# Optimization experiments

Measured on AMD Instinct MI355X. Metric: run time of the kernel, lower is better.

Reference implementation:

```python
import jax, jax.numpy as jnp
import numpy as np

NBITS = 8
REDUCE = 64
OUT = 512


def setup_inputs() -> dict:
    key = jax.random.key(0)
    ks = jax.random.split(key, 6)
    T, B, C = 512, 16, 512
    ne = 2 ** NBITS
    x = jax.random.normal(ks[0], (T, B, C), dtype=jnp.float32)
    key_in = jax.random.normal(ks[1], (T, B, C), dtype=jnp.float32)  # unused by forward (overwritten)
    # xavier-ish init scales
    map_w = jax.random.normal(ks[2], (NBITS, C), dtype=jnp.float32) * np.sqrt(2.0 / (C + NBITS))
    map_b = jnp.zeros((NBITS,), dtype=jnp.float32)
    pw_w1 = jax.random.normal(ks[3], (REDUCE, C), dtype=jnp.float32) * np.sqrt(2.0 / (C + REDUCE))
    pw_w21 = jax.random.normal(ks[4], (ne, OUT * REDUCE), dtype=jnp.float32) * np.sqrt(2.0 / (ne + OUT * REDUCE))
    pw_w22 = jax.random.normal(ks[5], (ne, OUT * REDUCE), dtype=jnp.float32) * np.sqrt(2.0 / (ne + OUT * REDUCE))
    pw_B = jnp.zeros((1, 1, OUT), dtype=jnp.float32)
    return {"x": x, "key": key_in, "map_w": map_w, "map_b": map_b,
            "pw_w1": pw_w1, "pw_w21": pw_w21, "pw_w22": pw_w22, "pw_B": pw_B}


def reference(x, key, map_w, map_b, pw_w1, pw_w21, pw_w22, pw_B):
    # x: (T,B,C). `key` arg is overwritten by x in the original source.
    T, B, C = x.shape
    nbits = map_w.shape[0]
    out_dim = pw_B.shape[-1]
    reduce_dim = pw_w1.shape[0]

    k = x.reshape(T * B, C) @ map_w.T + map_b          # (T*B, nbits)
    z = jnp.clip(1.2 * jax.nn.sigmoid(k) - 0.1, 0.0, 1.0)  # saturated sigmoid
    code = (z > 0.5).astype(z.dtype)                   # eval: hard binary code

    pows = (2 ** jnp.arange(nbits, dtype=jnp.int32))   # bit_to_int weights
    qz1 = jnp.sum(code.astype(jnp.int32) * pows, axis=-1)          # (T*B,)
    qz2 = jnp.sum((1 - code.astype(jnp.int32)) * pows, axis=-1)    # (T*B,)

    # gather per-token expert rows and synthesize per-token weight matrix
    w2 = (pw_w21[qz1] + pw_w22[qz2]).reshape(T, B, out_dim, reduce_dim)

    # original computes (w2 @ pw_w1) @ x; reassociated as w2 @ (pw_w1 @ x)
    # to avoid materializing the (T,B,out,in) intermediate (same math)
    v = jnp.einsum('ri,tbi->tbr', pw_w1, x)            # (T,B,reduce)
    y = jnp.einsum('tbor,tbr->tbo', w2, v) + pw_B      # (T,B,out)

    loss = jnp.zeros((1,), dtype=x.dtype)
    return (y, loss)
```

## Files before the change

kernel.cpp:

```cpp
#include <hip/hip_runtime.h>

#define NTOK 8192
#define CDIM 512
#define NB   8
#define RD   64
#define OD   512
#define XROW 516

typedef unsigned char  u8;
typedef unsigned int   u32;
typedef unsigned short u16;

#define WS_Q      0
#define WS_COUNTS 8192
#define WS_CURSOR 9216
#define WS_OFF    10240
#define WS_LIST   11520
#define WS_V      28672
#define WS_NEED   (WS_V + NTOK * RD * 4)

__global__ __launch_bounds__(256) void kInit(u32* __restrict__ counts) {
    counts[threadIdx.x] = 0u;
}

__global__ __launch_bounds__(256) void kA(
    const float* __restrict__ x, const float* __restrict__ map_w,
    const float* __restrict__ map_b, const float* __restrict__ w1,
    u8* __restrict__ q_out, float* __restrict__ v_out,
    u32* __restrict__ counts, float* __restrict__ loss_out)
{
    const int t    = threadIdx.x;
    const int tok0 = blockIdx.x * 16;
    __shared__ float xs[16 * XROW];

    const float4* __restrict__ xsrc = (const float4*)(x + (size_t)tok0 * CDIM);
    #pragma unroll
    for (int u = 0; u < 8; ++u) {
        int i = u * 256 + t;
        int r = i >> 7, c = i & 127;
        *(float4*)(xs + r * XROW + c * 4) = xsrc[i];
    }
    __syncthreads();

    const int wvu  = __builtin_amdgcn_readfirstlane(t >> 6);
    const int lane = t & 63;

    if (wvu < 2) {
        const int tb = tok0 + wvu * 8;
        const float4* __restrict__ w4  = (const float4*)w1 + (size_t)lane * 128;
        const float4* __restrict__ xg  = (const float4*)x + (size_t)tb * 128;
        float a0=0.f,a1=0.f,a2=0.f,a3=0.f,a4=0.f,a5=0.f,a6=0.f,a7=0.f;
        for (int k = 0; k < 128; ++k) {
            float4 w = w4[k];
            float4 x0 = xg[0*128+k], x1 = xg[1*128+k], x2 = xg[2*128+k], x3 = xg[3*128+k];
            float4 x4v = xg[4*128+k], x5 = xg[5*128+k], x6 = xg[6*128+k], x7 = xg[7*128+k];
            a0 += w.x*x0.x + w.y*x0.y + w.z*x0.z + w.w*x0.w;
            a1 += w.x*x1.x + w.y*x1.y + w.z*x1.z + w.w*x1.w;
            a2 += w.x*x2.x + w.y*x2.y + w.z*x2.z + w.w*x2.w;
            a3 += w.x*x3.x + w.y*x3.y + w.z*x3.z + w.w*x3.w;
            a4 += w.x*x4v.x + w.y*x4v.y + w.z*x4v.z + w.w*x4v.w;
            a5 += w.x*x5.x + w.y*x5.y + w.z*x5.z + w.w*x5.w;
            a6 += w.x*x6.x + w.y*x6.y + w.z*x6.z + w.w*x6.w;
            a7 += w.x*x7.x + w.y*x7.y + w.z*x7.z + w.w*x7.w;
        }
        v_out[(size_t)(tb+0) * RD + lane] = a0;
        v_out[(size_t)(tb+1) * RD + lane] = a1;
        v_out[(size_t)(tb+2) * RD + lane] = a2;
        v_out[(size_t)(tb+3) * RD + lane] = a3;
        v_out[(size_t)(tb+4) * RD + lane] = a4;
        v_out[(size_t)(tb+5) * RD + lane] = a5;
        v_out[(size_t)(tb+6) * RD + lane] = a6;
        v_out[(size_t)(tb+7) * RD + lane] = a7;
    } else {
        const int lt  = t - 128;
        const int tk  = lt >> 3;
        const int bit = lt & 7;
        const float4* __restrict__ m4 = (const float4*)map_w + (size_t)bit * 128;
        const float4* __restrict__ xl = (const float4*)(xs + tk * XROW);
        double s = 0.0;
        for (int k = 0; k < 128; ++k) {
            float4 m = m4[k], xv = xl[k];
            s += (double)m.x * (double)xv.x + (double)m.y * (double)xv.y
               + (double)m.z * (double)xv.z + (double)m.w * (double)xv.w;
        }
        s += (double)map_b[bit];
        unsigned long long mask = __ballot(s > 0.0);
        if (bit == 0) {
            u32 qv = (u32)((mask >> ((tk & 7) * 8)) & 0xFFull);
            q_out[tok0 + tk] = (u8)qv;
            atomicAdd(&counts[qv], 1u);
        }
    }
    if (blockIdx.x == 0 && t == 0) loss_out[0] = 0.0f;
}

__global__ __launch_bounds__(256) void kPrefix(
    const u32* __restrict__ counts, u32* __restrict__ off, u32* __restrict__ cursor)
{
    __shared__ u32 s[256];
    const int t = threadIdx.x;
    u32 c = counts[t];
    s[t] = c;
    __syncthreads();
    for (int d = 1; d < 256; d <<= 1) {
        u32 v = (t >= d) ? s[t - d] : 0u;
        __syncthreads();
        s[t] += v;
        __syncthreads();
    }
    u32 excl = s[t] - c;
    off[t] = excl;
    cursor[t] = excl;
    if (t == 255) off[256] = s[255];
}

__global__ __launch_bounds__(256) void kScatter(
    const u8* __restrict__ q_arr, u32* __restrict__ cursor, u16* __restrict__ list)
{
    const int tok = blockIdx.x * 256 + threadIdx.x;
    u32 pos = atomicAdd(&cursor[q_arr[tok]], 1u);
    list[pos] = (u16)tok;
}

__global__ __launch_bounds__(256) void kB(
    const u16* __restrict__ list, const u32* __restrict__ off,
    const float* __restrict__ v_arr,
    const float* __restrict__ w21, const float* __restrict__ w22,
    const float* __restrict__ pwB, float* __restrict__ y)
{
    const int q  = blockIdx.x >> 2;
    const int oh = (blockIdx.x >> 1) & 1;
    const int th = blockIdx.x & 1;
    const int t  = threadIdx.x;
    const int o  = oh * 256 + t;

    const u32 lo = off[q], hi = off[q + 1];
    const int n = (int)(hi - lo);
    if (n == 0) return;
    const int half = (n + 1) >> 1;
    const int s0   = th * half;
    const int cnt  = min(n - s0, half);
    if (cnt <= 0) return;

    __shared__ u16 ltok[4096];
    for (int i = t; i < cnt; i += 256) ltok[i] = list[lo + s0 + i];

    const float4* __restrict__ pa = (const float4*)(w21 + ((size_t)q * OD + o) * RD);
    const float4* __restrict__ pb = (const float4*)(w22 + ((size_t)(255 - q) * OD + o) * RD);
    float4 w[16];
    #pragma unroll
    for (int j = 0; j < 16; ++j) {
        float4 a = pa[j], b = pb[j];
        w[j] = make_float4(a.x + b.x, a.y + b.y, a.z + b.z, a.w + b.w);
    }
    const float bias = pwB[o];
    __syncthreads();

    const float4* __restrict__ v4 = (const float4*)v_arr;
    for (int i = 0; i < cnt; i += 4) {
        const int nb = cnt - i;
        const int i1 = (nb > 1) ? i + 1 : i;
        const int i2 = (nb > 2) ? i + 2 : i;
        const int i3 = (nb > 3) ? i + 3 : i;
        const int t0 = __builtin_amdgcn_readfirstlane((int)ltok[i]);
        const int t1 = __builtin_amdgcn_readfirstlane((int)ltok[i1]);
        const int t2 = __builtin_amdgcn_readfirstlane((int)ltok[i2]);
        const int t3 = __builtin_amdgcn_readfirstlane((int)ltok[i3]);
        const float4* __restrict__ p0 = v4 + (size_t)t0 * 16;
        const float4* __restrict__ p1 = v4 + (size_t)t1 * 16;
        const float4* __restrict__ p2 = v4 + (size_t)t2 * 16;
        const float4* __restrict__ p3 = v4 + (size_t)t3 * 16;
        float a0 = bias, a1 = bias, a2 = bias, a3 = bias;
        #pragma unroll
        for (int j = 0; j < 16; ++j) {
            float4 ww = w[j];
            float4 v0 = p0[j]; a0 += ww.x*v0.x + ww.y*v0.y + ww.z*v0.z + ww.w*v0.w;
            float4 v1 = p1[j]; a1 += ww.x*v1.x + ww.y*v1.y + ww.z*v1.z + ww.w*v1.w;
            float4 v2 = p2[j]; a2 += ww.x*v2.x + ww.y*v2.y + ww.z*v2.z + ww.w*v2.w;
            float4 v3 = p3[j]; a3 += ww.x*v3.x + ww.y*v3.y + ww.z*v3.z + ww.w*v3.w;
        }
        y[(size_t)t0 * OD + o] = a0;
        if (nb > 1) y[(size_t)t1 * OD + o] = a1;
        if (nb > 2) y[(size_t)t2 * OD + o] = a2;
        if (nb > 3) y[(size_t)t3 * OD + o] = a3;
    }
}

__global__ __launch_bounds__(256) void mono(
    const float* __restrict__ x, const float* __restrict__ map_w,
    const float* __restrict__ map_b, const float* __restrict__ w1,
    const float* __restrict__ w21, const float* __restrict__ w22,
    const float* __restrict__ pwB, float* __restrict__ y)
{
    const int tok = blockIdx.x;
    const int t   = threadIdx.x;
    __shared__ float xsh[CDIM];
    __shared__ float vsh[RD];
    __shared__ int qsh;

    if (t == 0) qsh = 0;
    for (int i = t; i < CDIM; i += 256) xsh[i] = x[(size_t)tok * CDIM + i];
    __syncthreads();

    if (t < NB) {
        double a = 0.0;
        const float* mrow = map_w + (size_t)t * CDIM;
        for (int j = 0; j < CDIM; ++j) a += (double)mrow[j] * (double)xsh[j];
        a += (double)map_b[t];
        if (a > 0.0) atomicOr(&qsh, 1 << t);
    }
    if (t < RD) {
        const float* wrow = w1 + (size_t)t * CDIM;
        float acc = 0.f;
        for (int j = 0; j < CDIM; ++j) acc += wrow[j] * xsh[j];
        vsh[t] = acc;
    }
    __syncthreads();

    const int q = qsh;
    for (int o = t; o < OD; o += 256) {
        const float* pa = w21 + (size_t)q * (OD * RD) + (size_t)o * RD;
        const float* pb = w22 + (size_t)(255 - q) * (OD * RD) + (size_t)o * RD;
        float acc = pwB[o];
        for (int r = 0; r < RD; ++r) acc += (pa[r] + pb[r]) * vsh[r];
        y[(size_t)tok * OD + o] = acc;
    }
    if (tok == 0 && t == 0) y[(size_t)NTOK * OD] = 0.0f;
}

extern "C" void kernel_launch(void* const* d_in, const int* in_sizes, int n_in,
                              void* d_out, int out_size, void* d_ws, size_t ws_size,
                              hipStream_t stream) {
    const float* x     = (const float*)d_in[0];
    const float* map_w = (const float*)d_in[2];
    const float* map_b = (const float*)d_in[3];
    const float* w1    = (const float*)d_in[4];
    const float* w21   = (const float*)d_in[5];
    const float* w22   = (const float*)d_in[6];
    const float* pwB   = (const float*)d_in[7];
    float* out = (float*)d_out;

    if (ws_size >= (size_t)WS_NEED) {
        char* ws = (char*)d_ws;
        u8*    q_ws   = (u8*)(ws + WS_Q);
        u32*   counts = (u32*)(ws + WS_COUNTS);
        u32*   cursor = (u32*)(ws + WS_CURSOR);
        u32*   off    = (u32*)(ws + WS_OFF);
        u16*   list   = (u16*)(ws + WS_LIST);
        float* v_ws   = (float*)(ws + WS_V);

        kInit<<<1, 256, 0, stream>>>(counts);
        kA<<<NTOK / 16, 256, 0, stream>>>(x, map_w, map_b, w1, q_ws, v_ws, counts,
                                          out + (size_t)NTOK * OD);
        kPrefix<<<1, 256, 0, stream>>>(counts, off, cursor);
        kScatter<<<NTOK / 256, 256, 0, stream>>>(q_ws, cursor, list);
        kB<<<1024, 256, 0, stream>>>(list, off, v_ws, w21, w22, pwB, out);
    } else {
        mono<<<NTOK, 256, 0, stream>>>(x, map_w, map_b, w1, w21, w22, pwB, out);
    }
}
```

Measured before the change: 223.4 us.

## Restructure projection kernel, merge histogram/scan/scatter into one sort kernel, reshape expert grid

The projection kernel now uses 512 threads with all 8 waves splitting both the w1 projection and the hash-code dot products. Each wave reads x from an XOR-swizzled shared tile and reduces its partial sums with cross-lane shuffles. The separate init, prefix and scatter kernels plus the global count atomics are replaced by a single one-block sort kernel that does the histogram, scan and scatter in shared memory. The expert kernel no longer splits tokens in halves, so it launches 512 blocks with a larger shared token list and issues weight loads early. This removes launches and global atomics, but serializes sorting in one block and gives uneven expert buckets less parallelism.

Result: slower. 232.9 us (+4.2%).

```diff
diff --git a/kernel.cpp b/kernel.cpp
--- a/kernel.cpp
+++ b/kernel.cpp
@@ -5,121 +5,125 @@
 #define NB   8
 #define RD   64
 #define OD   512
-#define XROW 516
 
 typedef unsigned char  u8;
 typedef unsigned int   u32;
 typedef unsigned short u16;
 
-#define WS_Q      0
-#define WS_COUNTS 8192
-#define WS_CURSOR 9216
-#define WS_OFF    10240
-#define WS_LIST   11520
-#define WS_V      28672
-#define WS_NEED   (WS_V + NTOK * RD * 4)
-
-__global__ __launch_bounds__(256) void kInit(u32* __restrict__ counts) {
-    counts[threadIdx.x] = 0u;
-}
-
-__global__ __launch_bounds__(256) void kA(
+#define WS_Q    0
+#define WS_OFF  8192
+#define WS_LIST 9728
+#define WS_V    26112
+#define WS_NEED (WS_V + (size_t)NTOK * RD * 4)
+
+__global__ __launch_bounds__(512) void kA(
     const float* __restrict__ x, const float* __restrict__ map_w,
     const float* __restrict__ map_b, const float* __restrict__ w1,
     u8* __restrict__ q_out, float* __restrict__ v_out,
-    u32* __restrict__ counts, float* __restrict__ loss_out)
+    float* __restrict__ loss_out)
 {
     const int t    = threadIdx.x;
     const int tok0 = blockIdx.x * 16;
-    __shared__ float xs[16 * XROW];
+    __shared__ float xs[16 * CDIM];
+    __shared__ float vs[16 * 68];
+    __shared__ u32   qm[8];
 
     const float4* __restrict__ xsrc = (const float4*)(x + (size_t)tok0 * CDIM);
     #pragma unroll
-    for (int u = 0; u < 8; ++u) {
-        int i = u * 256 + t;
-        int r = i >> 7, c = i & 127;
-        *(float4*)(xs + r * XROW + c * 4) = xsrc[i];
-    }
-    __syncthreads();
-
-    const int wvu  = __builtin_amdgcn_readfirstlane(t >> 6);
+    for (int u = 0; u < 4; ++u) {
+        int g  = u * 512 + t;
+        int r  = g >> 7, c4 = g & 127;
+        int col = (c4 * 4) ^ ((r & 7) << 3);
+        *(float4*)(xs + r * CDIM + col) = xsrc[g];
+    }
+    __syncthreads();
+
+    const int w    = t >> 6;
     const int lane = t & 63;
-
-    if (wvu < 2) {
-        const int tb = tok0 + wvu * 8;
-        const float4* __restrict__ w4  = (const float4*)w1 + (size_t)lane * 128;
-        const float4* __restrict__ xg  = (const float4*)x + (size_t)tb * 128;
-        float a0=0.f,a1=0.f,a2=0.f,a3=0.f,a4=0.f,a5=0.f,a6=0.f,a7=0.f;
-        for (int k = 0; k < 128; ++k) {
-            float4 w = w4[k];
-            float4 x0 = xg[0*128+k], x1 = xg[1*128+k], x2 = xg[2*128+k], x3 = xg[3*128+k];
-            float4 x4v = xg[4*128+k], x5 = xg[5*128+k], x6 = xg[6*128+k], x7 = xg[7*128+k];
-            a0 += w.x*x0.x + w.y*x0.y + w.z*x0.z + w.w*x0.w;
-            a1 += w.x*x1.x + w.y*x1.y + w.z*x1.z + w.w*x1.w;
-            a2 += w.x*x2.x + w.y*x2.y + w.z*x2.z + w.w*x2.w;
-            a3 += w.x*x3.x + w.y*x3.y + w.z*x3.z + w.w*x3.w;
-            a4 += w.x*x4v.x + w.y*x4v.y + w.z*x4v.z + w.w*x4v.w;
-            a5 += w.x*x5.x + w.y*x5.y + w.z*x5.z + w.w*x5.w;
-            a6 += w.x*x6.x + w.y*x6.y + w.z*x6.z + w.w*x6.w;
-            a7 += w.x*x7.x + w.y*x7.y + w.z*x7.z + w.w*x7.w;
+    const int tok  = lane & 15;
+    const int ch   = lane >> 4;
+    const int sw   = (tok & 7) << 3;
+    const float* __restrict__ xrow = xs + tok * CDIM;
+    const float* __restrict__ wrow = w1 + (size_t)(w * 8) * CDIM;
+    const float* __restrict__ mrow = map_w + (size_t)w * CDIM;
+
+    float a[8] = {0.f, 0.f, 0.f, 0.f, 0.f, 0.f, 0.f, 0.f};
+    double s = 0.0;
+
+    for (int st = 0; st < 32; ++st) {
+        const int c = ch * 128 + st * 4;
+        float4 xv = *(const float4*)(xrow + (c ^ sw));
+        #pragma unroll
+        for (int j = 0; j < 8; ++j) {
+            float4 wv = *(const float4*)(wrow + (size_t)j * CDIM + c);
+            a[j] += wv.x * xv.x + wv.y * xv.y + wv.z * xv.z + wv.w * xv.w;
         }
-        v_out[(size_t)(tb+0) * RD + lane] = a0;
-        v_out[(size_t)(tb+1) * RD + lane] = a1;
-        v_out[(size_t)(tb+2) * RD + lane] = a2;
-        v_out[(size_t)(tb+3) * RD + lane] = a3;
-        v_out[(size_t)(tb+4) * RD + lane] = a4;
-        v_out[(size_t)(tb+5) * RD + lane] = a5;
-        v_out[(size_t)(tb+6) * RD + lane] = a6;
-        v_out[(size_t)(tb+7) * RD + lane] = a7;
-    } else {
-        const int lt  = t - 128;
-        const int tk  = lt >> 3;
-        const int bit = lt & 7;
-        const float4* __restrict__ m4 = (const float4*)map_w + (size_t)bit * 128;
-        const float4* __restrict__ xl = (const float4*)(xs + tk * XROW);
-        double s = 0.0;
-        for (int k = 0; k < 128; ++k) {
-            float4 m = m4[k], xv = xl[k];
-            s += (double)m.x * (double)xv.x + (double)m.y * (double)xv.y
-               + (double)m.z * (double)xv.z + (double)m.w * (double)xv.w;
-        }
-        s += (double)map_b[bit];
-        unsigned long long mask = __ballot(s > 0.0);
-        if (bit == 0) {
-            u32 qv = (u32)((mask >> ((tk & 7) * 8)) & 0xFFull);
-            q_out[tok0 + tk] = (u8)qv;
-            atomicAdd(&counts[qv], 1u);
-        }
+        float4 mv = *(const float4*)(mrow + c);
+        s += (double)mv.x * (double)xv.x + (double)mv.y * (double)xv.y
+           + (double)mv.z * (double)xv.z + (double)mv.w * (double)xv.w;
+    }
+
+    #pragma unroll
+    for (int j = 0; j < 8; ++j) {
+        a[j] += __shfl_xor(a[j], 16);
+        a[j] += __shfl_xor(a[j], 32);
+    }
+    s += __shfl_xor(s, 16);
+    s += __shfl_xor(s, 32);
+    s += (double)map_b[w];
+
+    unsigned long long mask = __ballot(s > 0.0);
+    if (lane == 0) qm[w] = (u32)(mask & 0xFFFFull);
+
+    if (lane < 16) {
+        #pragma unroll
+        for (int j = 0; j < 8; ++j) vs[tok * 68 + w * 8 + j] = a[j];
+    }
+    __syncthreads();
+
+    if (t < 16) {
+        u32 q = 0;
+        #pragma unroll
+        for (int b = 0; b < 8; ++b) q |= ((qm[b] >> t) & 1u) << b;
+        q_out[tok0 + t] = (u8)q;
+    }
+    if (t < 256) {
+        int tk = t >> 4, j4 = t & 15;
+        *(float4*)(v_out + (size_t)(tok0 + tk) * RD + j4 * 4) =
+            *(const float4*)(vs + tk * 68 + j4 * 4);
     }
     if (blockIdx.x == 0 && t == 0) loss_out[0] = 0.0f;
 }
 
-__global__ __launch_bounds__(256) void kPrefix(
-    const u32* __restrict__ counts, u32* __restrict__ off, u32* __restrict__ cursor)
-{
-    __shared__ u32 s[256];
+__global__ __launch_bounds__(1024) void kSort(
+    const u8* __restrict__ q_arr, u32* __restrict__ off, u16* __restrict__ list)
+{
+    __shared__ u32 hist[256], curs[256], scan[256];
     const int t = threadIdx.x;
-    u32 c = counts[t];
-    s[t] = c;
+    if (t < 256) hist[t] = 0u;
+    __syncthreads();
+    for (int i = t; i < NTOK; i += 1024) atomicAdd(&hist[q_arr[i]], 1u);
+    __syncthreads();
+    if (t < 256) scan[t] = hist[t];
     __syncthreads();
     for (int d = 1; d < 256; d <<= 1) {
-        u32 v = (t >= d) ? s[t - d] : 0u;
+        u32 v = 0u;
+        if (t < 256 && t >= d) v = scan[t - d];
         __syncthreads();
-        s[t] += v;
+        if (t < 256) scan[t] += v;
         __syncthreads();
     }
-    u32 excl = s[t] - c;
-    off[t] = excl;
-    cursor[t] = excl;
-    if (t == 255) off[256] = s[255];
-}
-
-__global__ __launch_bounds__(256) void kScatter(
-    const u8* __restrict__ q_arr, u32* __restrict__ cursor, u16* __restrict__ list)
-{
-    const int tok = blockIdx.x * 256 + threadIdx.x;
-    u32 pos = atomicAdd(&cursor[q_arr[tok]], 1u);
-    list[pos] = (u16)tok;
+    if (t < 256) {
+        u32 excl = scan[t] - hist[t];
+        curs[t] = excl;
+        off[t]  = excl;
+        if (t == 255) off[256] = scan[255];
+    }
+    __syncthreads();
+    for (int i = t; i < NTOK; i += 1024) {
+        u32 pos = atomicAdd(&curs[q_arr[i]], 1u);
+        list[pos] = (u16)i;
+    }
 }
 
 __global__ __launch_bounds__(256) void kB(
@@ -128,44 +132,41 @@
     const float* __restrict__ w21, const float* __restrict__ w22,
     const float* __restrict__ pwB, float* __restrict__ y)
 {
-    const int q  = blockIdx.x >> 2;
-    const int oh = (blockIdx.x >> 1) & 1;
-    const int th = blockIdx.x & 1;
+    const int q  = blockIdx.x >> 1;
+    const int oh = blockIdx.x & 1;
     const int t  = threadIdx.x;
     const int o  = oh * 256 + t;
-
     const u32 lo = off[q], hi = off[q + 1];
-    const int n = (int)(hi - lo);
+    const int n  = (int)(hi - lo);
     if (n == 0) return;
-    const int half = (n + 1) >> 1;
-    const int s0   = th * half;
-    const int cnt  = min(n - s0, half);
-    if (cnt <= 0) return;
-
-    __shared__ u16 ltok[4096];
-    for (int i = t; i < cnt; i += 256) ltok[i] = list[lo + s0 + i];
+
+    __shared__ u16 ltok[NTOK];
 
     const float4* __restrict__ pa = (const float4*)(w21 + ((size_t)q * OD + o) * RD);
     const float4* __restrict__ pb = (const float4*)(w22 + ((size_t)(255 - q) * OD + o) * RD);
+    float4 wa[16], wb[16];
+    #pragma unroll
+    for (int j = 0; j < 16; ++j) wa[j] = pa[j];
+    #pragma unroll
+    for (int j = 0; j < 16; ++j) wb[j] = pb[j];
+
+    for (int i = t; i < n; i += 256) ltok[i] = list[lo + i];
+
     float4 w[16];
     #pragma unroll
-    for (int j = 0; j < 16; ++j) {
-        float4 a = pa[j], b = pb[j];
-        w[j] = make_float4(a.x + b.x, a.y + b.y, a.z + b.z, a.w + b.w);
-    }
+    for (int j = 0; j < 16; ++j)
+        w[j] = make_float4(wa[j].x + wb[j].x, wa[j].y + wb[j].y,
+                           wa[j].z + wb[j].z, wa[j].w + wb[j].w);
     const float bias = pwB[o];
     __syncthreads();
 
     const float4* __restrict__ v4 = (const float4*)v_arr;
-    for (int i = 0; i < cnt; i += 4) {
-        const int nb = cnt - i;
-        const int i1 = (nb > 1) ? i + 1 : i;
-        const int i2 = (nb > 2) ? i + 2 : i;
-        const int i3 = (nb > 3) ? i + 3 : i;
-        const int t0 = __builtin_amdgcn_readfirstlane((int)ltok[i]);
-        const int t1 = __builtin_amdgcn_readfirstlane((int)ltok[i1]);
-        const int t2 = __builtin_amdgcn_readfirstlane((int)ltok[i2]);
-        const int t3 = __builtin_amdgcn_readfirstlane((int)ltok[i3]);
+    for (int i = 0; i < n; i += 4) {
+        const int nb = n - i;
+        const int t0 = (int)ltok[i];
+        const int t1 = (int)ltok[(nb > 1) ? i + 1 : i];
+        const int t2 = (int)ltok[(nb > 2) ? i + 2 : i];
+        const int t3 = (int)ltok[(nb > 3) ? i + 3 : i];
         const float4* __restrict__ p0 = v4 + (size_t)t0 * 16;
         const float4* __restrict__ p1 = v4 + (size_t)t1 * 16;
         const float4* __restrict__ p2 = v4 + (size_t)t2 * 16;
@@ -240,21 +241,17 @@
     const float* pwB   = (const float*)d_in[7];
     float* out = (float*)d_out;
 
-    if (ws_size >= (size_t)WS_NEED) {
+    if (ws_size >= WS_NEED) {
         char* ws = (char*)d_ws;
         u8*    q_ws   = (u8*)(ws + WS_Q);
-        u32*   counts = (u32*)(ws + WS_COUNTS);
-        u32*   cursor = (u32*)(ws + WS_CURSOR);
         u32*   off    = (u32*)(ws + WS_OFF);
         u16*   list   = (u16*)(ws + WS_LIST);
         float* v_ws   = (float*)(ws + WS_V);
 
-        kInit<<<1, 256, 0, stream>>>(counts);
-        kA<<<NTOK / 16, 256, 0, stream>>>(x, map_w, map_b, w1, q_ws, v_ws, counts,
+        kA<<<NTOK / 16, 512, 0, stream>>>(x, map_w, map_b, w1, q_ws, v_ws,
                                           out + (size_t)NTOK * OD);
-        kPrefix<<<1, 256, 0, stream>>>(counts, off, cursor);
-        kScatter<<<NTOK / 256, 256, 0, stream>>>(q_ws, cursor, list);
-        kB<<<1024, 256, 0, stream>>>(list, off, v_ws, w21, w22, pwB, out);
+        kSort<<<1, 1024, 0, stream>>>(q_ws, off, list);
+        kB<<<512, 256, 0, stream>>>(list, off, v_ws, w21, w22, pwB, out);
     } else {
         mono<<<NTOK, 256, 0, stream>>>(x, map_w, map_b, w1, w21, w22, pwB, out);
     }
```
